# Performance work log

Hardware: AMD Instinct MI355X
Metric: run time of the kernel (lower is better)

The kernel has to match this reference:

```python
import jax, jax.numpy as jnp
import numpy as np

QLEN, MLEN, BSZ = 1024, 1024, 4
D_MODEL, N_HEAD, D_HEAD, D_INNER = 1024, 16, 64, 4096
KLEN = QLEN + MLEN  # = rlen
LN_EPS = 1e-5


def setup_inputs() -> dict:
    key = jax.random.key(0)
    ks = jax.random.split(key, 16)
    s = 0.02
    nhd = N_HEAD * D_HEAD
    inp = {
        "dec_inp": jax.random.normal(ks[0], (QLEN, BSZ, D_MODEL), jnp.float32),
        "r": jax.random.normal(ks[1], (KLEN, D_MODEL), jnp.float32),
        "r_w_bias": jax.random.normal(ks[2], (N_HEAD, D_HEAD), jnp.float32) * s,
        "r_r_bias": jax.random.normal(ks[3], (N_HEAD, D_HEAD), jnp.float32) * s,
        "mems": jax.random.normal(ks[4], (MLEN, BSZ, D_MODEL), jnp.float32),
        # causal mask with memory: position j visible to query i iff j <= i + MLEN
        "dec_attn_mask": (jnp.arange(KLEN)[None, :] > (jnp.arange(QLEN)[:, None] + MLEN))[:, :, None],
        # parameters
        "qkv_w": jax.random.normal(ks[5], (D_MODEL, 3 * nhd), jnp.float32) * s,
        "r_w": jax.random.normal(ks[6], (D_MODEL, nhd), jnp.float32) * s,
        "o_w": jax.random.normal(ks[7], (nhd, D_MODEL), jnp.float32) * s,
        "ln1_w": jnp.ones((D_MODEL,), jnp.float32),
        "ln1_b": jnp.zeros((D_MODEL,), jnp.float32),
        "ln2_w": jnp.ones((D_MODEL,), jnp.float32),
        "ln2_b": jnp.zeros((D_MODEL,), jnp.float32),
        "ff_w1": jax.random.normal(ks[8], (D_MODEL, D_INNER), jnp.float32) * s,
        "ff_b1": jnp.zeros((D_INNER,), jnp.float32),
        "ff_w2": jax.random.normal(ks[9], (D_INNER, D_MODEL), jnp.float32) * s,
        "ff_b2": jnp.zeros((D_MODEL,), jnp.float32),
    }
    return inp


def _layer_norm(x, w, b):
    mu = jnp.mean(x, axis=-1, keepdims=True)
    var = jnp.mean(jnp.square(x - mu), axis=-1, keepdims=True)
    return (x - mu) * jax.lax.rsqrt(var + LN_EPS) * w + b


def _rel_shift(x):
    # x: [qlen, rlen, bsz, n_head] -- Transformer-XL pad/reshape shift
    q, rl = x.shape[0], x.shape[1]
    zero_pad = jnp.zeros((q, 1) + x.shape[2:], x.dtype)
    x_padded = jnp.concatenate([zero_pad, x], axis=1)
    x_padded = x_padded.reshape((rl + 1, q) + x.shape[2:])
    return x_padded[1:].reshape(x.shape)


def reference(dec_inp, r, r_w_bias, r_r_bias, mems, dec_attn_mask,
              qkv_w, r_w, o_w, ln1_w, ln1_b, ln2_w, ln2_b,
              ff_w1, ff_b1, ff_w2, ff_b2):
    qlen, bsz = dec_inp.shape[0], dec_inp.shape[1]
    nhd = N_HEAD * D_HEAD
    scale = 1.0 / (D_HEAD ** 0.5)

    cat = jnp.concatenate([mems, dec_inp], axis=0)          # [klen, b, d]
    w_heads = cat @ qkv_w                                   # [klen, b, 3*nhd]
    w_head_q, w_head_k, w_head_v = jnp.split(w_heads, 3, axis=-1)
    w_head_q = w_head_q[-qlen:]                             # [qlen, b, nhd]
    klen = w_head_k.shape[0]

    w_head_q = w_head_q.reshape(qlen, bsz, N_HEAD, D_HEAD)
    w_head_k = w_head_k.reshape(klen, bsz, N_HEAD, D_HEAD)
    w_head_v = w_head_v.reshape(klen, bsz, N_HEAD, D_HEAD)
    r_head_k = (r @ r_w).reshape(-1, N_HEAD, D_HEAD)        # [rlen, n, d]

    AC = jnp.einsum('ibnd,jbnd->ijbn', w_head_q + r_w_bias, w_head_k)
    BD = jnp.einsum('ibnd,jnd->ijbn', w_head_q + r_r_bias, r_head_k)
    BD = _rel_shift(BD)

    attn_score = (AC + BD) * scale                          # [q, k, b, n]
    attn_score = jnp.where(dec_attn_mask[:, :, :, None], -jnp.inf, attn_score)
    attn_prob = jax.nn.softmax(attn_score, axis=1)

    attn_vec = jnp.einsum('ijbn,jbnd->ibnd', attn_prob, w_head_v)
    attn_out = attn_vec.reshape(qlen, bsz, nhd) @ o_w       # [q, b, d]

    output = _layer_norm(dec_inp + attn_out, ln1_w, ln1_b)
    ff = jax.nn.relu(output @ ff_w1 + ff_b1) @ ff_w2 + ff_b2
    return _layer_norm(output + ff, ln2_w, ln2_b)
```

## Files before the change

kernel.cpp:

```cpp
#include <hip/hip_runtime.h>
#include <hip/hip_bf16.h>
#include <math.h>

#define QLEN 1024
#define MLEN 1024
#define BSZ 4
#define KLEN 2048
#define NH 16
#define DH 64
#define DM 1024
#define DI 4096
#define NHD 1024
#define LN_EPS 1e-5f

typedef short bf16x8 __attribute__((ext_vector_type(8)));
typedef float f32x4 __attribute__((ext_vector_type(4)));
typedef unsigned int uint4v __attribute__((ext_vector_type(4)));

__device__ __forceinline__ float bf2f(unsigned short u) {
    union { unsigned u32; float f; } x; x.u32 = ((unsigned)u) << 16; return x.f;
}
__device__ __forceinline__ unsigned short f2bf(float f) {
    __hip_bfloat16 h = __float2bfloat16(f);
    return *(unsigned short*)&h;
}

static const size_t OFF_CATB  = 0;
static const size_t OFF_VTG   = 0;
static const size_t OFF_WHB   = 16777216;
static const size_t OFF_RB    = 67108864;
static const size_t OFF_RHKB  = 71303168;
static const size_t OFF_AVB   = 75497472;
static const size_t OFF_TMP   = 83886080;
static const size_t OFF_LN1F  = 100663296;
static const size_t OFF_LN1B  = 117440512;
static const size_t OFF_FFHB  = 125829120;
static const size_t OFF_QKVWT = 159383552;
static const size_t OFF_RWT   = 165675008;
static const size_t OFF_OWT   = 167772160;
static const size_t OFF_FFW1T = 169869312;
static const size_t OFF_FFW2T = 178257920;
static const size_t OFF_BK    = 186646528;
static const size_t OFF_BR    = 187170816;

__global__ __launch_bounds__(256) void cast_cat(const float* __restrict__ mems,
                                                const float* __restrict__ dec,
                                                unsigned short* __restrict__ out) {
    size_t i8 = ((size_t)blockIdx.x * 256 + threadIdx.x) * 8;
    const size_t half = (size_t)MLEN * BSZ * DM;
    const float* src = (i8 < half) ? (mems + i8) : (dec + (i8 - half));
    float4 v0 = *(const float4*)src;
    float4 v1 = *(const float4*)(src + 4);
    ushort4 o0 = {f2bf(v0.x), f2bf(v0.y), f2bf(v0.z), f2bf(v0.w)};
    ushort4 o1 = {f2bf(v1.x), f2bf(v1.y), f2bf(v1.z), f2bf(v1.w)};
    *(ushort4*)&out[i8] = o0;
    *(ushort4*)&out[i8 + 4] = o1;
}

__global__ __launch_bounds__(256) void cast_f32_bf16(const float* __restrict__ in,
                                                     unsigned short* __restrict__ out) {
    size_t i8 = ((size_t)blockIdx.x * 256 + threadIdx.x) * 8;
    float4 v0 = *(const float4*)(in + i8);
    float4 v1 = *(const float4*)(in + i8 + 4);
    ushort4 o0 = {f2bf(v0.x), f2bf(v0.y), f2bf(v0.z), f2bf(v0.w)};
    ushort4 o1 = {f2bf(v1.x), f2bf(v1.y), f2bf(v1.z), f2bf(v1.w)};
    *(ushort4*)&out[i8] = o0;
    *(ushort4*)&out[i8 + 4] = o1;
}

__global__ __launch_bounds__(256) void transpose_cast_all(
        const float* __restrict__ qkv_w, const float* __restrict__ r_w,
        const float* __restrict__ o_w,  const float* __restrict__ ff_w1,
        const float* __restrict__ ff_w2,
        unsigned short* __restrict__ qkvwT, unsigned short* __restrict__ rwT,
        unsigned short* __restrict__ owT, unsigned short* __restrict__ ffw1T,
        unsigned short* __restrict__ ffw2T) {
    __shared__ float tile[32][33];
    const int bid = blockIdx.x;
    const float* in; unsigned short* out; int K, N, nx, lid;
    if (bid < 3072)      { in = qkv_w; out = qkvwT; K = 1024; N = 3072; nx = 96;  lid = bid; }
    else if (bid < 4096) { in = r_w;   out = rwT;   K = 1024; N = 1024; nx = 32;  lid = bid - 3072; }
    else if (bid < 5120) { in = o_w;   out = owT;   K = 1024; N = 1024; nx = 32;  lid = bid - 4096; }
    else if (bid < 9216) { in = ff_w1; out = ffw1T; K = 1024; N = 4096; nx = 128; lid = bid - 5120; }
    else                 { in = ff_w2; out = ffw2T; K = 4096; N = 1024; nx = 32;  lid = bid - 9216; }
    const int n0 = (lid % nx) * 32;
    const int k0 = (lid / nx) * 32;
    const int t = threadIdx.x;
    const int r = t >> 3;
    const int c0 = (t & 7) << 2;
    float4 v = *(const float4*)&in[(size_t)(k0 + r) * N + n0 + c0];
    tile[r][c0 + 0] = v.x; tile[r][c0 + 1] = v.y;
    tile[r][c0 + 2] = v.z; tile[r][c0 + 3] = v.w;
    __syncthreads();
    ushort4 o = {f2bf(tile[c0 + 0][r]), f2bf(tile[c0 + 1][r]),
                 f2bf(tile[c0 + 2][r]), f2bf(tile[c0 + 3][r])};
    *(ushort4*)&out[(size_t)(n0 + r) * K + k0 + c0] = o;
}

__global__ __launch_bounds__(256) void gemm_bf16(const unsigned short* __restrict__ A,
                                                 const unsigned short* __restrict__ Bt,
                                                 const float* __restrict__ bias,
                                                 void* __restrict__ C,
                                                 int M, int N, int K, int flags) {
    __shared__ __align__(16) unsigned short As[128 * 64];
    __shared__ __align__(16) unsigned short Bs[128 * 64];

    const int tid = threadIdx.x;
    const int w = tid >> 6, l = tid & 63;
    const int wr = w >> 1, wc = w & 1;
    const int row0 = blockIdx.y * 128;
    const int col0 = blockIdx.x * 128;

    f32x4 acc[4][4] = {};

    uint4v ra[4], rb[4];
    {
#pragma unroll
        for (int q = 0; q < 4; ++q) {
            int f = q * 256 + tid, r = f >> 3, c = f & 7;
            ra[q] = *(const uint4v*)&A[(size_t)(row0 + r) * K + c * 8];
            rb[q] = *(const uint4v*)&Bt[(size_t)(col0 + r) * K + c * 8];
        }
    }

    const int nt = K >> 6;
    for (int kt = 0; kt < nt; ++kt) {
        __syncthreads();
#pragma unroll
        for (int q = 0; q < 4; ++q) {
            int f = q * 256 + tid, r = f >> 3, c = f & 7;
            int sw = (c ^ (r & 7)) << 3;
            *(uint4v*)&As[r * 64 + sw] = ra[q];
            *(uint4v*)&Bs[r * 64 + sw] = rb[q];
        }
        __syncthreads();
        if (kt + 1 < nt) {
            const int k0 = (kt + 1) << 6;
#pragma unroll
            for (int q = 0; q < 4; ++q) {
                int f = q * 256 + tid, r = f >> 3, c = f & 7;
                ra[q] = *(const uint4v*)&A[(size_t)(row0 + r) * K + k0 + c * 8];
                rb[q] = *(const uint4v*)&Bt[(size_t)(col0 + r) * K + k0 + c * 8];
            }
        }
#pragma unroll
        for (int ks = 0; ks < 2; ++ks) {
            bf16x8 a[4], bfr[4];
#pragma unroll
            for (int m = 0; m < 4; ++m) {
                int arow = wr * 64 + m * 16 + (l & 15);
                int chunk = (ks * 4 + (l >> 4)) ^ (arow & 7);
                a[m] = *(const bf16x8*)&As[arow * 64 + chunk * 8];
            }
#pragma unroll
            for (int n = 0; n < 4; ++n) {
                int brow = wc * 64 + n * 16 + (l & 15);
                int chunk = (ks * 4 + (l >> 4)) ^ (brow & 7);
                bfr[n] = *(const bf16x8*)&Bs[brow * 64 + chunk * 8];
            }
#pragma unroll
            for (int m = 0; m < 4; ++m)
#pragma unroll
                for (int n = 0; n < 4; ++n)
                    acc[m][n] = __builtin_amdgcn_mfma_f32_16x16x32_bf16(a[m], bfr[n], acc[m][n], 0, 0, 0);
        }
    }

#pragma unroll
    for (int n = 0; n < 4; ++n) {
        const int ccol = col0 + wc * 64 + n * 16 + (l & 15);
        const float bv = (flags & 1) ? bias[ccol] : 0.0f;
#pragma unroll
        for (int m = 0; m < 4; ++m) {
            const int crow0 = row0 + wr * 64 + m * 16 + ((l >> 4) << 2);
#pragma unroll
            for (int reg = 0; reg < 4; ++reg) {
                float v = acc[m][n][reg] + bv;
                if (flags & 2) v = fmaxf(v, 0.0f);
                if (flags & 4)
                    ((unsigned short*)C)[(size_t)(crow0 + reg) * N + ccol] = f2bf(v);
                else
                    ((float*)C)[(size_t)(crow0 + reg) * N + ccol] = v;
            }
        }
    }
}

__global__ __launch_bounds__(256) void vtrans(const unsigned short* __restrict__ whb,
                                              unsigned short* __restrict__ vtg) {
    __shared__ unsigned short tile[64][72];
    const int bn = blockIdx.y;
    const int b = bn >> 4, n = bn & 15, nb = n * 64;
    const int jt0 = blockIdx.x * 64;
    const int tid = threadIdx.x;
#pragma unroll
    for (int g = 0; g < 2; ++g) {
        int f = g * 256 + tid;
        int key = f >> 3, c = f & 7;
        uint4v v = *(const uint4v*)&whb[((size_t)(jt0 + key) * 4 + b) * 3072 + 2048 + nb + c * 8];
        *(uint4v*)&tile[key][c * 8] = v;
    }
    __syncthreads();
#pragma unroll
    for (int g = 0; g < 2; ++g) {
        int f = g * 256 + tid;
        int d = f >> 3, ck = f & 7;
        unsigned short tmp[8];
#pragma unroll
        for (int e = 0; e < 8; ++e) tmp[e] = tile[ck * 8 + e][d];
        *(uint4v*)&vtg[(size_t)bn * 131072 + (size_t)d * 2048 + jt0 + ck * 8] = *(uint4v*)tmp;
    }
}

__global__ __launch_bounds__(256) void bias_kernel(const unsigned short* __restrict__ whb,
                                                   const unsigned short* __restrict__ rhkb,
                                                   const float* __restrict__ r_w_bias,
                                                   const float* __restrict__ r_r_bias,
                                                   float* __restrict__ bias_k,
                                                   float* __restrict__ bias_r) {
    int id = blockIdx.x * 256 + threadIdx.x;
    if (id < 64 * 2048) {
        int bn = id >> 11, j = id & 2047;
        int b = bn >> 4, n = bn & 15;
        const unsigned short* kp = &whb[((size_t)j * 4 + b) * 3072 + 1024 + n * 64];
        const float* wb = &r_w_bias[n * 64];
        float acc = 0.f;
#pragma unroll
        for (int d = 0; d < 64; ++d) acc += wb[d] * bf2f(kp[d]);
        bias_k[id] = acc * 0.125f;
    } else {
        int id2 = id - 64 * 2048;
        if (id2 < 16 * 2048) {
            int n = id2 >> 11, rel = id2 & 2047;
            const unsigned short* rp = &rhkb[(size_t)rel * 1024 + n * 64];
            const float* rb = &r_r_bias[n * 64];
            float acc = 0.f;
#pragma unroll
            for (int d = 0; d < 64; ++d) acc += rb[d] * bf2f(rp[d]);
            bias_r[id2] = acc * 0.125f;
        }
    }
}

__global__ __launch_bounds__(512) void flash_attn_mfma(const unsigned short* __restrict__ whb,
                                                       const unsigned short* __restrict__ rhkb,
                                                       const unsigned short* __restrict__ vtg,
                                                       const float* __restrict__ bias_k,
                                                       const float* __restrict__ bias_r,
                                                       unsigned short* __restrict__ avb) {
    const int bid = blockIdx.x;
    const int bn = bid >> 3;
    const int z = bid & 7;
    const int bx = (z & 1) ? (z >> 1) : 7 - (z >> 1);
    const int b = bn >> 4, n = bn & 15, nb = n * 64;
    const int i0 = bx << 7;
    const int tid = threadIdx.x;
    const int wq = tid >> 6;
    const int lane = tid & 63;
    const int rg = lane >> 4;
    const int lc = lane & 15;

    __shared__ __align__(16) unsigned short Ks[4096];
    __shared__ __align__(16) unsigned short Rs[16384];
    __shared__ __align__(16) unsigned short Vt[4096];
    __shared__ __align__(16) unsigned short Ps[8][1024];

    bf16x8 qf[2];
    {
        const int qrow = MLEN + i0 + wq * 16 + lc;
        const unsigned short* qp = whb + ((size_t)qrow * 4 + b) * 3072 + nb + rg * 8;
        bf16x8 q0 = *(const bf16x8*)(qp);
        bf16x8 q1 = *(const bf16x8*)(qp + 32);
#pragma unroll
        for (int e = 0; e < 8; ++e) {
            unsigned short u0 = (unsigned short)q0[e];
            unsigned short u1 = (unsigned short)q1[e];
            qf[0][e] = (short)(((u0 & 0x7F80) > 0x0180) ? (unsigned short)(u0 - 0x0180)
                                                        : (unsigned short)(u0 & 0x8000));
            qf[1][e] = (short)(((u1 & 0x7F80) > 0x0180) ? (unsigned short)(u1 - 0x0180)
                                                        : (unsigned short)(u1 & 0x8000));
        }
    }

    f32x4 Oacc[4] = {};
    float mrun[4] = {-INFINITY, -INFINITY, -INFINITY, -INFINITY};
    float lrun[4] = {0.f, 0.f, 0.f, 0.f};

    const int ntiles = 2 * bx + 18;
    const int wbase_off = 112 - 16 * wq;

    const int srow = tid >> 3;
    const int sc = tid & 7;

    int srcl[4];
    bool hi5[4];
#pragma unroll
    for (int r = 0; r < 4; ++r) {
        const int qr = rg * 4 + r;
        srcl[r] = (rg << 4) | ((15 + lc - qr) & 15);
        hi5[r] = (lc > qr);
    }

    uint4v pk, pv, pr3[3];
    {
        pk = *(const uint4v*)&whb[((size_t)srow * 4 + b) * 3072 + 1024 + nb + sc * 8];
        pv = *(const uint4v*)&vtg[(size_t)bn * 131072 + (size_t)srow * 2048 + sc * 8];
        const int relbase0 = 896 - i0;
#pragma unroll
        for (int p = 0; p < 3; ++p) {
            const int a = relbase0 + p * 64 + srow;
            pr3[p] = *(const uint4v*)&rhkb[(size_t)a * 1024 + nb + sc * 8];
        }
    }

    for (int kt = 0; kt < ntiles; ++kt) {
        const int jt0 = kt << 6;
        const int relbase = jt0 - i0 + 896;
        __syncthreads();

        *(uint4v*)&Ks[srow * 64 + ((sc ^ (srow & 7)) << 3)] = pk;
        *(uint4v*)&Vt[srow * 64 + ((sc ^ (srow & 7)) << 3)] = pv;
        if (kt == 0) {
#pragma unroll
            for (int p = 0; p < 3; ++p) {
                const int a = relbase + p * 64 + srow;
                const int dst = ((a >> 6) & 3) * 4096 + (a & 63) * 64 + ((sc ^ (a & 7)) << 3);
                *(uint4v*)&Rs[dst] = pr3[p];
            }
        } else {
            const int a = relbase + 128 + srow;
            const int dst = ((a >> 6) & 3) * 4096 + (a & 63) * 64 + ((sc ^ (a & 7)) << 3);
            *(uint4v*)&Rs[dst] = pr3[0];
        }
        if (kt + 1 < ntiles) {
            const int jn = jt0 + 64;
            pk = *(const uint4v*)&whb[((size_t)(jn + srow) * 4 + b) * 3072 + 1024 + nb + sc * 8];
            pv = *(const uint4v*)&vtg[(size_t)bn * 131072 + (size_t)srow * 2048 + jn + sc * 8];
            int a = relbase + 192 + srow;
            if (a > 2047) a = 2047;
            pr3[0] = *(const uint4v*)&rhkb[(size_t)a * 1024 + nb + sc * 8];
        }
        __syncthreads();

        f32x4 Sacc[4];
        __builtin_amdgcn_s_setprio(1);
#pragma unroll
        for (int nf = 0; nf < 4; ++nf) {
            const int key = nf * 16 + lc;
            const int c7 = key & 7;
            const bf16x8 kf0 = *(const bf16x8*)&Ks[key * 64 + ((rg ^ c7) << 3)];
            const bf16x8 kf1 = *(const bf16x8*)&Ks[key * 64 + (((4 + rg) ^ c7) << 3)];
            f32x4 zz = {0.f, 0.f, 0.f, 0.f};
            zz = __builtin_amdgcn_mfma_f32_16x16x32_bf16(qf[0], kf0, zz, 0, 0, 0);
            Sacc[nf] = __builtin_amdgcn_mfma_f32_16x16x32_bf16(qf[1], kf1, zz, 0, 0, 0);
        }
        __builtin_amdgcn_s_setprio(0);

        const int wbase = relbase + wbase_off;
        const bool needmask = (wbase + 78 > 2047);
        float sv[4][4];
        float tmax[4] = {-INFINITY, -INFINITY, -INFINITY, -INFINITY};

        f32x4 bdpA;
        {
            const int a = wbase + lc;
            const int rbase = ((a >> 6) & 3) * 4096 + (a & 63) * 64;
            const int c7 = a & 7;
            const bf16x8 rf0 = *(const bf16x8*)&Rs[rbase + ((rg ^ c7) << 3)];
            const bf16x8 rf1 = *(const bf16x8*)&Rs[rbase + (((4 + rg) ^ c7) << 3)];
            f32x4 bd = {0.f, 0.f, 0.f, 0.f};
            bd = __builtin_amdgcn_mfma_f32_16x16x32_bf16(qf[0], rf0, bd, 0, 0, 0);
            bd = __builtin_amdgcn_mfma_f32_16x16x32_bf16(qf[1], rf1, bd, 0, 0, 0);
            const int aa = a > 2047 ? 2047 : a;
            const float brv = bias_r[n * 2048 + aa];
#pragma unroll
            for (int r = 0; r < 4; ++r) bdpA[r] = bd[r] + brv;
        }
#pragma unroll
        for (int nf = 0; nf < 4; ++nf) {
            f32x4 bdpB;
            {
                const int a = wbase + (nf + 1) * 16 + lc;
                const int rbase = ((a >> 6) & 3) * 4096 + (a & 63) * 64;
                const int c7 = a & 7;
                const bf16x8 rf0 = *(const bf16x8*)&Rs[rbase + ((rg ^ c7) << 3)];
                const bf16x8 rf1 = *(const bf16x8*)&Rs[rbase + (((4 + rg) ^ c7) << 3)];
                f32x4 bd = {0.f, 0.f, 0.f, 0.f};
                bd = __builtin_amdgcn_mfma_f32_16x16x32_bf16(qf[0], rf0, bd, 0, 0, 0);
                bd = __builtin_amdgcn_mfma_f32_16x16x32_bf16(qf[1], rf1, bd, 0, 0, 0);
                const int aa = a > 2047 ? 2047 : a;
                const float brv = bias_r[n * 2048 + aa];
#pragma unroll
                for (int r = 0; r < 4; ++r) bdpB[r] = bd[r] + brv;
            }
            const int jl = nf * 16 + lc;
            const float bkv = bias_k[(size_t)bn * 2048 + jt0 + jl];
#pragma unroll
            for (int r = 0; r < 4; ++r) {
                const float v0 = __shfl(bdpA[r], srcl[r]);
                const float v1 = __shfl(bdpB[r], srcl[r]);
                const float bdv = hi5[r] ? v1 : v0;
                float s = Sacc[nf][r] + bkv + bdv;
                if (needmask) {
                    const int qr = rg * 4 + r;
                    s = (wbase + 15 + jl - qr <= 2047) ? s : -INFINITY;
                }
                sv[nf][r] = s;
                tmax[r] = fmaxf(tmax[r], s);
            }
            bdpA = bdpB;
        }

        float ef[4];
#pragma unroll
        for (int r = 0; r < 4; ++r) {
            float tm = tmax[r];
            tm = fmaxf(tm, __shfl_xor(tm, 1));
            tm = fmaxf(tm, __shfl_xor(tm, 2));
            tm = fmaxf(tm, __shfl_xor(tm, 4));
            tm = fmaxf(tm, __shfl_xor(tm, 8));
            const float mn = fmaxf(mrun[r], tm);
            ef[r] = __expf(mrun[r] - mn);
            mrun[r] = mn;
        }
        unsigned short* ps = &Ps[wq][0];
        float rsum[4] = {0.f, 0.f, 0.f, 0.f};
#pragma unroll
        for (int nf = 0; nf < 4; ++nf) {
            const int jl = nf * 16 + lc;
#pragma unroll
            for (int r = 0; r < 4; ++r) {
                const int qr = rg * 4 + r;
                const float p = __expf(sv[nf][r] - mrun[r]);
                rsum[r] += p;
                ps[qr * 64 + (((jl >> 3) ^ (qr & 7)) << 3) + (jl & 7)] = f2bf(p);
            }
        }
#pragma unroll
        for (int r = 0; r < 4; ++r) {
            float rs = rsum[r];
            rs += __shfl_xor(rs, 1);
            rs += __shfl_xor(rs, 2);
            rs += __shfl_xor(rs, 4);
            rs += __shfl_xor(rs, 8);
            lrun[r] = lrun[r] * ef[r] + rs;
        }
        const int need_rescale = (ef[0] < 1.f) | (ef[1] < 1.f) | (ef[2] < 1.f) | (ef[3] < 1.f);
        if (__any(need_rescale)) {
#pragma unroll
            for (int nf = 0; nf < 4; ++nf)
#pragma unroll
                for (int r = 0; r < 4; ++r) Oacc[nf][r] *= ef[r];
        }

        {
            const int c7 = lc & 7;
            const bf16x8 pf0 = *(const bf16x8*)&ps[lc * 64 + ((rg ^ c7) << 3)];
            const bf16x8 pf1 = *(const bf16x8*)&ps[lc * 64 + (((4 + rg) ^ c7) << 3)];
            __builtin_amdgcn_s_setprio(1);
#pragma unroll
            for (int nf = 0; nf < 4; ++nf) {
                const int d = nf * 16 + lc;
                const int d7 = d & 7;
                const bf16x8 vf0 = *(const bf16x8*)&Vt[d * 64 + ((rg ^ d7) << 3)];
                const bf16x8 vf1 = *(const bf16x8*)&Vt[d * 64 + (((4 + rg) ^ d7) << 3)];
                Oacc[nf] = __builtin_amdgcn_mfma_f32_16x16x32_bf16(pf0, vf0, Oacc[nf], 0, 0, 0);
                Oacc[nf] = __builtin_amdgcn_mfma_f32_16x16x32_bf16(pf1, vf1, Oacc[nf], 0, 0, 0);
            }
            __builtin_amdgcn_s_setprio(0);
        }
    }

    float inv[4];
#pragma unroll
    for (int r = 0; r < 4; ++r) inv[r] = 1.0f / lrun[r];
#pragma unroll
    for (int nf = 0; nf < 4; ++nf) {
        const int d = nf * 16 + lc;
#pragma unroll
        for (int r = 0; r < 4; ++r) {
            const int iq = i0 + wq * 16 + rg * 4 + r;
            avb[((size_t)iq * 4 + b) * 1024 + nb + d] = f2bf(Oacc[nf][r] * inv[r]);
        }
    }
}

__global__ __launch_bounds__(256) void add_ln_kernel(const float* __restrict__ a,
                                                     const float* __restrict__ b,
                                                     const float* __restrict__ w,
                                                     const float* __restrict__ bias,
                                                     float* __restrict__ out,
                                                     unsigned short* __restrict__ out_bf) {
    const int row = blockIdx.x;
    const int t = threadIdx.x;
    __shared__ float xs[DM];
    __shared__ float red[256];

    const float* ar = a + (size_t)row * DM;
    const float* br = b + (size_t)row * DM;

    float lsum = 0.f;
#pragma unroll
    for (int c = t; c < DM; c += 256) {
        float v = ar[c] + br[c];
        xs[c] = v;
        lsum += v;
    }
    red[t] = lsum;
    __syncthreads();
    for (int off = 128; off > 0; off >>= 1) {
        if (t < off) red[t] += red[t + off];
        __syncthreads();
    }
    const float mu = red[0] * (1.0f / DM);
    __syncthreads();

    float lvar = 0.f;
#pragma unroll
    for (int c = t; c < DM; c += 256) {
        float dv = xs[c] - mu;
        lvar += dv * dv;
    }
    red[t] = lvar;
    __syncthreads();
    for (int off = 128; off > 0; off >>= 1) {
        if (t < off) red[t] += red[t + off];
        __syncthreads();
    }
    const float rstd = rsqrtf(red[0] * (1.0f / DM) + LN_EPS);
    __syncthreads();

    float* orow = out + (size_t)row * DM;
#pragma unroll
    for (int c = t; c < DM; c += 256) {
        float v = (xs[c] - mu) * rstd * w[c] + bias[c];
        orow[c] = v;
        if (out_bf) out_bf[(size_t)row * DM + c] = f2bf(v);
    }
}

extern "C" void kernel_launch(void* const* d_in, const int* in_sizes, int n_in,
                              void* d_out, int out_size, void* d_ws, size_t ws_size,
                              hipStream_t stream) {
    const float* dec_inp  = (const float*)d_in[0];
    const float* r        = (const float*)d_in[1];
    const float* r_w_bias = (const float*)d_in[2];
    const float* r_r_bias = (const float*)d_in[3];
    const float* mems     = (const float*)d_in[4];
    const float* qkv_w    = (const float*)d_in[6];
    const float* r_w      = (const float*)d_in[7];
    const float* o_w      = (const float*)d_in[8];
    const float* ln1_w    = (const float*)d_in[9];
    const float* ln1_b    = (const float*)d_in[10];
    const float* ln2_w    = (const float*)d_in[11];
    const float* ln2_b    = (const float*)d_in[12];
    const float* ff_w1    = (const float*)d_in[13];
    const float* ff_b1    = (const float*)d_in[14];
    const float* ff_w2    = (const float*)d_in[15];
    const float* ff_b2    = (const float*)d_in[16];
    float* out = (float*)d_out;
    char* ws = (char*)d_ws;

    unsigned short* catb  = (unsigned short*)(ws + OFF_CATB);
    unsigned short* vtg   = (unsigned short*)(ws + OFF_VTG);
    unsigned short* whb   = (unsigned short*)(ws + OFF_WHB);
    unsigned short* rb    = (unsigned short*)(ws + OFF_RB);
    unsigned short* rhkb  = (unsigned short*)(ws + OFF_RHKB);
    unsigned short* avb   = (unsigned short*)(ws + OFF_AVB);
    float*          tmp   = (float*)(ws + OFF_TMP);
    float*          ln1f  = (float*)(ws + OFF_LN1F);
    unsigned short* ln1b  = (unsigned short*)(ws + OFF_LN1B);
    unsigned short* ffhb  = (unsigned short*)(ws + OFF_FFHB);
    unsigned short* qkvwT = (unsigned short*)(ws + OFF_QKVWT);
    unsigned short* rwT   = (unsigned short*)(ws + OFF_RWT);
    unsigned short* owT   = (unsigned short*)(ws + OFF_OWT);
    unsigned short* ffw1T = (unsigned short*)(ws + OFF_FFW1T);
    unsigned short* ffw2T = (unsigned short*)(ws + OFF_FFW2T);
    float*          bk    = (float*)(ws + OFF_BK);
    float*          brr   = (float*)(ws + OFF_BR);

    cast_cat<<<dim3(4096), 256, 0, stream>>>(mems, dec_inp, catb);
    cast_f32_bf16<<<dim3(1024), 256, 0, stream>>>(r, rb);
    transpose_cast_all<<<dim3(13312), 256, 0, stream>>>(
        qkv_w, r_w, o_w, ff_w1, ff_w2, qkvwT, rwT, owT, ffw1T, ffw2T);

    gemm_bf16<<<dim3(24, 64), 256, 0, stream>>>(catb, qkvwT, nullptr, whb,
                                                KLEN * BSZ, 3 * NHD, DM, 4);
    gemm_bf16<<<dim3(8, 16), 256, 0, stream>>>(rb, rwT, nullptr, rhkb,
                                               KLEN, NHD, DM, 4);

    vtrans<<<dim3(32, 64), 256, 0, stream>>>(whb, vtg);
    bias_kernel<<<dim3(640), 256, 0, stream>>>(whb, rhkb, r_w_bias, r_r_bias, bk, brr);

    flash_attn_mfma<<<dim3(512), 512, 0, stream>>>(
        whb, rhkb, vtg, bk, brr, avb);

    gemm_bf16<<<dim3(8, 32), 256, 0, stream>>>(avb, owT, nullptr, tmp,
                                               QLEN * BSZ, DM, NHD, 0);
    add_ln_kernel<<<dim3(QLEN * BSZ), 256, 0, stream>>>(
        dec_inp, tmp, ln1_w, ln1_b, ln1f, ln1b);
    gemm_bf16<<<dim3(32, 32), 256, 0, stream>>>(ln1b, ffw1T, ff_b1, ffhb,
                                                QLEN * BSZ, DI, DM, 1 | 2 | 4);
    gemm_bf16<<<dim3(8, 32), 256, 0, stream>>>(ffhb, ffw2T, ff_b2, tmp,
                                               QLEN * BSZ, DM, DI, 1);
    add_ln_kernel<<<dim3(QLEN * BSZ), 256, 0, stream>>>(
        ln1f, tmp, ln2_w, ln2_b, out, nullptr);
}
```

Measured before the change: 444.6 us.

## Fold positional biases into query and transpose MFMA operands in attention

Drops the separate bias kernel and its precomputed key/rel bias arrays. The attention kernel now builds two biased, pre-scaled query fragments (q+r_w_bias and q+r_r_bias) and swaps MFMA operand order so each lane owns one query row. That ownership removes the per-row shuffle reductions and lets the rel-shift of BD go through a per-wave LDS scratch buffer instead of cross-lane shuffles. Adding the bias in bf16 before the dot product changes rounding slightly. It also does five BD MFMA groups through LDS per tile, which adds shared-memory traffic.

```diff
diff --git a/kernel.cpp b/kernel.cpp
--- a/kernel.cpp
+++ b/kernel.cpp
@@ -40,8 +40,6 @@
 static const size_t OFF_OWT   = 167772160;
 static const size_t OFF_FFW1T = 169869312;
 static const size_t OFF_FFW2T = 178257920;
-static const size_t OFF_BK    = 186646528;
-static const size_t OFF_BR    = 187170816;
 
 __global__ __launch_bounds__(256) void cast_cat(const float* __restrict__ mems,
                                                 const float* __restrict__ dec,
@@ -212,41 +210,11 @@
     }
 }
 
-__global__ __launch_bounds__(256) void bias_kernel(const unsigned short* __restrict__ whb,
-                                                   const unsigned short* __restrict__ rhkb,
-                                                   const float* __restrict__ r_w_bias,
-                                                   const float* __restrict__ r_r_bias,
-                                                   float* __restrict__ bias_k,
-                                                   float* __restrict__ bias_r) {
-    int id = blockIdx.x * 256 + threadIdx.x;
-    if (id < 64 * 2048) {
-        int bn = id >> 11, j = id & 2047;
-        int b = bn >> 4, n = bn & 15;
-        const unsigned short* kp = &whb[((size_t)j * 4 + b) * 3072 + 1024 + n * 64];
-        const float* wb = &r_w_bias[n * 64];
-        float acc = 0.f;
-#pragma unroll
-        for (int d = 0; d < 64; ++d) acc += wb[d] * bf2f(kp[d]);
-        bias_k[id] = acc * 0.125f;
-    } else {
-        int id2 = id - 64 * 2048;
-        if (id2 < 16 * 2048) {
-            int n = id2 >> 11, rel = id2 & 2047;
-            const unsigned short* rp = &rhkb[(size_t)rel * 1024 + n * 64];
-            const float* rb = &r_r_bias[n * 64];
-            float acc = 0.f;
-#pragma unroll
-            for (int d = 0; d < 64; ++d) acc += rb[d] * bf2f(rp[d]);
-            bias_r[id2] = acc * 0.125f;
-        }
-    }
-}
-
 __global__ __launch_bounds__(512) void flash_attn_mfma(const unsigned short* __restrict__ whb,
                                                        const unsigned short* __restrict__ rhkb,
                                                        const unsigned short* __restrict__ vtg,
-                                                       const float* __restrict__ bias_k,
-                                                       const float* __restrict__ bias_r,
+                                                       const float* __restrict__ r_w_bias,
+                                                       const float* __restrict__ r_r_bias,
                                                        unsigned short* __restrict__ avb) {
     const int bid = blockIdx.x;
     const int bn = bid >> 3;
@@ -259,47 +227,41 @@
     const int lane = tid & 63;
     const int rg = lane >> 4;
     const int lc = lane & 15;
+    const int m7 = lc & 7;
 
     __shared__ __align__(16) unsigned short Ks[4096];
     __shared__ __align__(16) unsigned short Rs[16384];
     __shared__ __align__(16) unsigned short Vt[4096];
-    __shared__ __align__(16) unsigned short Ps[8][1024];
-
-    bf16x8 qf[2];
+    __shared__ __align__(16) unsigned short SCR[8][1280];
+
+    bf16x8 qac0, qac1, qbd0, qbd1;
     {
         const int qrow = MLEN + i0 + wq * 16 + lc;
         const unsigned short* qp = whb + ((size_t)qrow * 4 + b) * 3072 + nb + rg * 8;
         bf16x8 q0 = *(const bf16x8*)(qp);
         bf16x8 q1 = *(const bf16x8*)(qp + 32);
+        const float* wbp = r_w_bias + nb + rg * 8;
+        const float* rbp = r_r_bias + nb + rg * 8;
 #pragma unroll
         for (int e = 0; e < 8; ++e) {
-            unsigned short u0 = (unsigned short)q0[e];
-            unsigned short u1 = (unsigned short)q1[e];
-            qf[0][e] = (short)(((u0 & 0x7F80) > 0x0180) ? (unsigned short)(u0 - 0x0180)
-                                                        : (unsigned short)(u0 & 0x8000));
-            qf[1][e] = (short)(((u1 & 0x7F80) > 0x0180) ? (unsigned short)(u1 - 0x0180)
-                                                        : (unsigned short)(u1 & 0x8000));
+            const float v0 = bf2f((unsigned short)q0[e]);
+            const float v1 = bf2f((unsigned short)q1[e]);
+            qac0[e] = (short)f2bf((v0 + wbp[e]) * 0.125f);
+            qbd0[e] = (short)f2bf((v0 + rbp[e]) * 0.125f);
+            qac1[e] = (short)f2bf((v1 + wbp[32 + e]) * 0.125f);
+            qbd1[e] = (short)f2bf((v1 + rbp[32 + e]) * 0.125f);
         }
     }
 
     f32x4 Oacc[4] = {};
-    float mrun[4] = {-INFINITY, -INFINITY, -INFINITY, -INFINITY};
-    float lrun[4] = {0.f, 0.f, 0.f, 0.f};
+    float mrun = -INFINITY, lrun = 0.f;
 
     const int ntiles = 2 * bx + 18;
     const int wbase_off = 112 - 16 * wq;
 
     const int srow = tid >> 3;
     const int sc = tid & 7;
-
-    int srcl[4];
-    bool hi5[4];
-#pragma unroll
-    for (int r = 0; r < 4; ++r) {
-        const int qr = rg * 4 + r;
-        srcl[r] = (rg << 4) | ((15 + lc - qr) & 15);
-        hi5[r] = (lc > qr);
-    }
+    unsigned short* scr = &SCR[wq][0];
 
     uint4v pk, pv, pr3[3];
     {
@@ -342,146 +304,102 @@
         }
         __syncthreads();
 
-        f32x4 Sacc[4];
+        f32x4 S[4];
         __builtin_amdgcn_s_setprio(1);
 #pragma unroll
         for (int nf = 0; nf < 4; ++nf) {
-            const int key = nf * 16 + lc;
-            const int c7 = key & 7;
-            const bf16x8 kf0 = *(const bf16x8*)&Ks[key * 64 + ((rg ^ c7) << 3)];
-            const bf16x8 kf1 = *(const bf16x8*)&Ks[key * 64 + (((4 + rg) ^ c7) << 3)];
+            const int row = nf * 16 + lc;
+            const bf16x8 kf0 = *(const bf16x8*)&Ks[row * 64 + ((rg ^ m7) << 3)];
+            const bf16x8 kf1 = *(const bf16x8*)&Ks[row * 64 + (((4 + rg) ^ m7) << 3)];
             f32x4 zz = {0.f, 0.f, 0.f, 0.f};
-            zz = __builtin_amdgcn_mfma_f32_16x16x32_bf16(qf[0], kf0, zz, 0, 0, 0);
-            Sacc[nf] = __builtin_amdgcn_mfma_f32_16x16x32_bf16(qf[1], kf1, zz, 0, 0, 0);
+            zz = __builtin_amdgcn_mfma_f32_16x16x32_bf16(kf0, qac0, zz, 0, 0, 0);
+            S[nf] = __builtin_amdgcn_mfma_f32_16x16x32_bf16(kf1, qac1, zz, 0, 0, 0);
         }
         __builtin_amdgcn_s_setprio(0);
 
         const int wbase = relbase + wbase_off;
+#pragma unroll
+        for (int g = 0; g < 5; ++g) {
+            const int a = wbase + g * 16 + lc;
+            const int rbase = ((a >> 6) & 3) * 4096 + (a & 63) * 64;
+            const bf16x8 rf0 = *(const bf16x8*)&Rs[rbase + ((rg ^ m7) << 3)];
+            const bf16x8 rf1 = *(const bf16x8*)&Rs[rbase + (((4 + rg) ^ m7) << 3)];
+            f32x4 bd = {0.f, 0.f, 0.f, 0.f};
+            bd = __builtin_amdgcn_mfma_f32_16x16x32_bf16(rf0, qbd0, bd, 0, 0, 0);
+            bd = __builtin_amdgcn_mfma_f32_16x16x32_bf16(rf1, qbd1, bd, 0, 0, 0);
+            ushort4 p4 = {f2bf(bd[0]), f2bf(bd[1]), f2bf(bd[2]), f2bf(bd[3])};
+            *(ushort4*)&scr[lc * 80 + g * 16 + rg * 4] = p4;
+        }
+
         const bool needmask = (wbase + 78 > 2047);
-        float sv[4][4];
-        float tmax[4] = {-INFINITY, -INFINITY, -INFINITY, -INFINITY};
-
-        f32x4 bdpA;
+        float tmax = -INFINITY;
+#pragma unroll
+        for (int nf = 0; nf < 4; ++nf) {
+#pragma unroll
+            for (int r = 0; r < 4; ++r) {
+                const int wb_ = 15 + nf * 16 + rg * 4 + r - lc;
+                float s = S[nf][r] + bf2f(scr[lc * 80 + wb_]);
+                if (needmask) s = (wbase + wb_ <= 2047) ? s : -INFINITY;
+                S[nf][r] = s;
+                tmax = fmaxf(tmax, s);
+            }
+        }
+
+        tmax = fmaxf(tmax, __shfl_xor(tmax, 16));
+        tmax = fmaxf(tmax, __shfl_xor(tmax, 32));
+        const float mn = fmaxf(mrun, tmax);
+        const float ef = __expf(mrun - mn);
+        mrun = mn;
+        float rsum = 0.f;
+#pragma unroll
+        for (int nf = 0; nf < 4; ++nf) {
+#pragma unroll
+            for (int r = 0; r < 4; ++r) {
+                const float p = __expf(S[nf][r] - mn);
+                S[nf][r] = p;
+                rsum += p;
+            }
+        }
+        rsum += __shfl_xor(rsum, 16);
+        rsum += __shfl_xor(rsum, 32);
+        lrun = lrun * ef + rsum;
+        if (__any(ef < 1.0f)) {
+#pragma unroll
+            for (int nf = 0; nf < 4; ++nf)
+#pragma unroll
+                for (int r = 0; r < 4; ++r) Oacc[nf][r] *= ef;
+        }
+
+#pragma unroll
+        for (int nf = 0; nf < 4; ++nf) {
+            ushort4 pw = {f2bf(S[nf][0]), f2bf(S[nf][1]), f2bf(S[nf][2]), f2bf(S[nf][3])};
+            const int chunk = nf * 2 + (rg >> 1);
+            *(ushort4*)&scr[lc * 80 + ((chunk ^ m7) << 3) + ((rg & 1) << 2)] = pw;
+        }
+
         {
-            const int a = wbase + lc;
-            const int rbase = ((a >> 6) & 3) * 4096 + (a & 63) * 64;
-            const int c7 = a & 7;
-            const bf16x8 rf0 = *(const bf16x8*)&Rs[rbase + ((rg ^ c7) << 3)];
-            const bf16x8 rf1 = *(const bf16x8*)&Rs[rbase + (((4 + rg) ^ c7) << 3)];
-            f32x4 bd = {0.f, 0.f, 0.f, 0.f};
-            bd = __builtin_amdgcn_mfma_f32_16x16x32_bf16(qf[0], rf0, bd, 0, 0, 0);
-            bd = __builtin_amdgcn_mfma_f32_16x16x32_bf16(qf[1], rf1, bd, 0, 0, 0);
-            const int aa = a > 2047 ? 2047 : a;
-            const float brv = bias_r[n * 2048 + aa];
-#pragma unroll
-            for (int r = 0; r < 4; ++r) bdpA[r] = bd[r] + brv;
-        }
-#pragma unroll
-        for (int nf = 0; nf < 4; ++nf) {
-            f32x4 bdpB;
-            {
-                const int a = wbase + (nf + 1) * 16 + lc;
-                const int rbase = ((a >> 6) & 3) * 4096 + (a & 63) * 64;
-                const int c7 = a & 7;
-                const bf16x8 rf0 = *(const bf16x8*)&Rs[rbase + ((rg ^ c7) << 3)];
-                const bf16x8 rf1 = *(const bf16x8*)&Rs[rbase + (((4 + rg) ^ c7) << 3)];
-                f32x4 bd = {0.f, 0.f, 0.f, 0.f};
-                bd = __builtin_amdgcn_mfma_f32_16x16x32_bf16(qf[0], rf0, bd, 0, 0, 0);
-                bd = __builtin_amdgcn_mfma_f32_16x16x32_bf16(qf[1], rf1, bd, 0, 0, 0);
-                const int aa = a > 2047 ? 2047 : a;
-                const float brv = bias_r[n * 2048 + aa];
-#pragma unroll
-                for (int r = 0; r < 4; ++r) bdpB[r] = bd[r] + brv;
-            }
-            const int jl = nf * 16 + lc;
-            const float bkv = bias_k[(size_t)bn * 2048 + jt0 + jl];
-#pragma unroll
-            for (int r = 0; r < 4; ++r) {
-                const float v0 = __shfl(bdpA[r], srcl[r]);
-                const float v1 = __shfl(bdpB[r], srcl[r]);
-                const float bdv = hi5[r] ? v1 : v0;
-                float s = Sacc[nf][r] + bkv + bdv;
-                if (needmask) {
-                    const int qr = rg * 4 + r;
-                    s = (wbase + 15 + jl - qr <= 2047) ? s : -INFINITY;
-                }
-                sv[nf][r] = s;
-                tmax[r] = fmaxf(tmax[r], s);
-            }
-            bdpA = bdpB;
-        }
-
-        float ef[4];
-#pragma unroll
-        for (int r = 0; r < 4; ++r) {
-            float tm = tmax[r];
-            tm = fmaxf(tm, __shfl_xor(tm, 1));
-            tm = fmaxf(tm, __shfl_xor(tm, 2));
-            tm = fmaxf(tm, __shfl_xor(tm, 4));
-            tm = fmaxf(tm, __shfl_xor(tm, 8));
-            const float mn = fmaxf(mrun[r], tm);
-            ef[r] = __expf(mrun[r] - mn);
-            mrun[r] = mn;
-        }
-        unsigned short* ps = &Ps[wq][0];
-        float rsum[4] = {0.f, 0.f, 0.f, 0.f};
-#pragma unroll
-        for (int nf = 0; nf < 4; ++nf) {
-            const int jl = nf * 16 + lc;
-#pragma unroll
-            for (int r = 0; r < 4; ++r) {
-                const int qr = rg * 4 + r;
-                const float p = __expf(sv[nf][r] - mrun[r]);
-                rsum[r] += p;
-                ps[qr * 64 + (((jl >> 3) ^ (qr & 7)) << 3) + (jl & 7)] = f2bf(p);
-            }
-        }
-#pragma unroll
-        for (int r = 0; r < 4; ++r) {
-            float rs = rsum[r];
-            rs += __shfl_xor(rs, 1);
-            rs += __shfl_xor(rs, 2);
-            rs += __shfl_xor(rs, 4);
-            rs += __shfl_xor(rs, 8);
-            lrun[r] = lrun[r] * ef[r] + rs;
-        }
-        const int need_rescale = (ef[0] < 1.f) | (ef[1] < 1.f) | (ef[2] < 1.f) | (ef[3] < 1.f);
-        if (__any(need_rescale)) {
-#pragma unroll
-            for (int nf = 0; nf < 4; ++nf)
-#pragma unroll
-                for (int r = 0; r < 4; ++r) Oacc[nf][r] *= ef[r];
-        }
-
-        {
-            const int c7 = lc & 7;
-            const bf16x8 pf0 = *(const bf16x8*)&ps[lc * 64 + ((rg ^ c7) << 3)];
-            const bf16x8 pf1 = *(const bf16x8*)&ps[lc * 64 + (((4 + rg) ^ c7) << 3)];
+            const bf16x8 pf0 = *(const bf16x8*)&scr[lc * 80 + ((rg ^ m7) << 3)];
+            const bf16x8 pf1 = *(const bf16x8*)&scr[lc * 80 + (((4 + rg) ^ m7) << 3)];
             __builtin_amdgcn_s_setprio(1);
 #pragma unroll
             for (int nf = 0; nf < 4; ++nf) {
-                const int d = nf * 16 + lc;
-                const int d7 = d & 7;
-                const bf16x8 vf0 = *(const bf16x8*)&Vt[d * 64 + ((rg ^ d7) << 3)];
-                const bf16x8 vf1 = *(const bf16x8*)&Vt[d * 64 + (((4 + rg) ^ d7) << 3)];
-                Oacc[nf] = __builtin_amdgcn_mfma_f32_16x16x32_bf16(pf0, vf0, Oacc[nf], 0, 0, 0);
-                Oacc[nf] = __builtin_amdgcn_mfma_f32_16x16x32_bf16(pf1, vf1, Oacc[nf], 0, 0, 0);
+                const int row = nf * 16 + lc;
+                const bf16x8 vf0 = *(const bf16x8*)&Vt[row * 64 + ((rg ^ m7) << 3)];
+                const bf16x8 vf1 = *(const bf16x8*)&Vt[row * 64 + (((4 + rg) ^ m7) << 3)];
+                Oacc[nf] = __builtin_amdgcn_mfma_f32_16x16x32_bf16(vf0, pf0, Oacc[nf], 0, 0, 0);
+                Oacc[nf] = __builtin_amdgcn_mfma_f32_16x16x32_bf16(vf1, pf1, Oacc[nf], 0, 0, 0);
             }
             __builtin_amdgcn_s_setprio(0);
         }
     }
 
-    float inv[4];
-#pragma unroll
-    for (int r = 0; r < 4; ++r) inv[r] = 1.0f / lrun[r];
+    const float inv = 1.0f / lrun;
+    const int qg = i0 + wq * 16 + lc;
 #pragma unroll
     for (int nf = 0; nf < 4; ++nf) {
-        const int d = nf * 16 + lc;
-#pragma unroll
-        for (int r = 0; r < 4; ++r) {
-            const int iq = i0 + wq * 16 + rg * 4 + r;
-            avb[((size_t)iq * 4 + b) * 1024 + nb + d] = f2bf(Oacc[nf][r] * inv[r]);
-        }
+        ushort4 o = {f2bf(Oacc[nf][0] * inv), f2bf(Oacc[nf][1] * inv),
+                     f2bf(Oacc[nf][2] * inv), f2bf(Oacc[nf][3] * inv)};
+        *(ushort4*)&avb[((size_t)qg * 4 + b) * 1024 + nb + nf * 16 + rg * 4] = o;
     }
 }
 
@@ -576,8 +494,6 @@
     unsigned short* owT   = (unsigned short*)(ws + OFF_OWT);
     unsigned short* ffw1T = (unsigned short*)(ws + OFF_FFW1T);
     unsigned short* ffw2T = (unsigned short*)(ws + OFF_FFW2T);
-    float*          bk    = (float*)(ws + OFF_BK);
-    float*          brr   = (float*)(ws + OFF_BR);
 
     cast_cat<<<dim3(4096), 256, 0, stream>>>(mems, dec_inp, catb);
     cast_f32_bf16<<<dim3(1024), 256, 0, stream>>>(r, rb);
@@ -590,10 +506,9 @@
                                                KLEN, NHD, DM, 4);
 
     vtrans<<<dim3(32, 64), 256, 0, stream>>>(whb, vtg);
-    bias_kernel<<<dim3(640), 256, 0, stream>>>(whb, rhkb, r_w_bias, r_r_bias, bk, brr);
 
     flash_attn_mfma<<<dim3(512), 512, 0, stream>>>(
-        whb, rhkb, vtg, bk, brr, avb);
+        whb, rhkb, vtg, r_w_bias, r_r_bias, avb);
 
     gemm_bf16<<<dim3(8, 32), 256, 0, stream>>>(avb, owT, nullptr, tmp,
                                                QLEN * BSZ, DM, NHD, 0);
```

Measured after the change: 421.7 us. 1.05x faster.
